# Kernel optimization log

Measured on AMD Instinct MI355X. Metric: run time of the kernel, lower is better.

The kernel has to match this reference:

```python
import jax, jax.numpy as jnp
import numpy as np
import math

D_MODEL = 1024
N_HEADS = 16
D_K = D_MODEL // N_HEADS
D_FF = 4096
B = 2
S = 2048
LN_EPS = 1e-3  # Keras LayerNormalization default


def setup_inputs() -> dict:
    key = jax.random.key(0)
    ks = jax.random.split(key, 16)
    s = 0.02
    inp = {
        "x": jax.random.normal(ks[0], (B, S, D_MODEL), dtype=jnp.float32),
        "weights": jax.random.uniform(ks[1], (B, S), dtype=jnp.float32),
        # attention projections (Dense: y = x @ W + b)
        "Wq": jax.random.normal(ks[2], (D_MODEL, D_MODEL), jnp.float32) * s,
        "bq": jnp.zeros((D_MODEL,), jnp.float32),
        "Wk": jax.random.normal(ks[3], (D_MODEL, D_MODEL), jnp.float32) * s,
        "bk": jnp.zeros((D_MODEL,), jnp.float32),
        "Wv": jax.random.normal(ks[4], (D_MODEL, D_MODEL), jnp.float32) * s,
        "bv": jnp.zeros((D_MODEL,), jnp.float32),
        "Wo": jax.random.normal(ks[5], (D_MODEL, D_MODEL), jnp.float32) * s,
        "bo": jnp.zeros((D_MODEL,), jnp.float32),
        # FFN
        "W1": jax.random.normal(ks[6], (D_MODEL, D_FF), jnp.float32) * s,
        "b1": jnp.zeros((D_FF,), jnp.float32),
        "W2": jax.random.normal(ks[7], (D_FF, D_MODEL), jnp.float32) * s,
        "b2": jnp.zeros((D_MODEL,), jnp.float32),
        # layer norms
        "g1": jnp.ones((D_MODEL,), jnp.float32),
        "be1": jnp.zeros((D_MODEL,), jnp.float32),
        "g2": jnp.ones((D_MODEL,), jnp.float32),
        "be2": jnp.zeros((D_MODEL,), jnp.float32),
    }
    return inp


def _layer_norm(x, gamma, beta):
    mu = jnp.mean(x, axis=-1, keepdims=True)
    var = jnp.mean(jnp.square(x - mu), axis=-1, keepdims=True)
    return (x - mu) * jax.lax.rsqrt(var + LN_EPS) * gamma + beta


def _block(x, weights, Wq, bq, Wk, bk, Wv, bv, Wo, bo, W1, b1, W2, b2, g1, be1, g2, be2):
    b, s, _ = x.shape
    # projections -> (B, H, S, d_k)
    def split_heads(y):
        return y.reshape(b, s, N_HEADS, D_K).transpose(0, 2, 1, 3)
    Q = split_heads(x @ Wq + bq)
    K = split_heads(x @ Wk + bk)
    V = split_heads(x @ Wv + bv)
    scores = jnp.einsum("bhqd,bhkd->bhqk", Q, K) / math.sqrt(D_K)
    log_w = jnp.log(weights + 1e-20)[:, None, None, :]  # (B,1,1,S)
    attn = jax.nn.softmax(scores + log_w, axis=-1)
    out = jnp.einsum("bhqk,bhkd->bhqd", attn, V)
    out = out.transpose(0, 2, 1, 3).reshape(b, s, D_MODEL)
    attn_out = out @ Wo + bo
    h = _layer_norm(x + attn_out, g1, be1)
    ffn = jax.nn.relu(h @ W1 + b1) @ W2 + b2
    return _layer_norm(h + ffn, g2, be2)


def reference(x, weights, Wq, bq, Wk, bk, Wv, bv, Wo, bo, W1, b1, W2, b2, g1, be1, g2, be2):
    return _block(x, weights, Wq, bq, Wk, bk, Wv, bv, Wo, bo, W1, b1, W2, b2, g1, be1, g2, be2)
```

## Files before the change

kernel.cpp:

```cpp
#include <hip/hip_runtime.h>
#include <cstdint>
#include <cstddef>

#define DM 1024
#define NH 16
#define DKH 64
#define DFF 4096
#define NB 2
#define SQL 2048
#define MROWS (NB * SQL)
#define QKVN 3072

typedef __attribute__((ext_vector_type(8))) __bf16 bf16x8;
typedef __attribute__((ext_vector_type(8))) short short8;
typedef __attribute__((ext_vector_type(4))) float f32x4;

__device__ __forceinline__ unsigned short f2bf(float f) {
    unsigned u = __float_as_uint(f);
    u += 0x7fffu + ((u >> 16) & 1u);
    return (unsigned short)(u >> 16);
}
__device__ __forceinline__ bf16x8 ldfrag(const unsigned short* p) {
    return __builtin_bit_cast(bf16x8, *(const short8*)p);
}
__device__ __forceinline__ void gl_lds16(const void* g, void* lds) {
    __builtin_amdgcn_global_load_lds(
        (const __attribute__((address_space(1))) unsigned int*)g,
        (__attribute__((address_space(3))) unsigned int*)lds, 16, 0, 0);
}
#define MFMA16(a, b, c) __builtin_amdgcn_mfma_f32_16x16x32_bf16(a, b, c, 0, 0, 0)

__global__ __launch_bounds__(256) void prep_misc(const float* __restrict__ x,
                                                 const float* __restrict__ wts,
                                                 const float* __restrict__ bq,
                                                 const float* __restrict__ bk,
                                                 const float* __restrict__ bv,
                                                 unsigned short* __restrict__ x_bf,
                                                 float* __restrict__ logw,
                                                 float* __restrict__ bqkv) {
    const int bid = blockIdx.x, tid = threadIdx.x;
    if (bid < 4096) {
        int i = (bid * 256 + tid) * 4;
        float4 v = *(const float4*)&x[i];
        ushort4 o;
        o.x = f2bf(v.x); o.y = f2bf(v.y); o.z = f2bf(v.z); o.w = f2bf(v.w);
        *(ushort4*)&x_bf[i] = o;
    } else if (bid < 4112) {
        int i = (bid - 4096) * 256 + tid;
        logw[i] = logf(wts[i] + 1e-20f);
    } else {
        int i = (bid - 4112) * 256 + tid;
        if (i < QKVN)
            bqkv[i] = i < 1024 ? bq[i] * 0.125f : (i < 2048 ? bk[i - 1024] : bv[i - 2048]);
    }
}

__global__ __launch_bounds__(256) void prep_weights(const float* __restrict__ Wq,
                                                    const float* __restrict__ Wk,
                                                    const float* __restrict__ Wv,
                                                    const float* __restrict__ Wo,
                                                    const float* __restrict__ W1,
                                                    unsigned short* __restrict__ wqkv_t,
                                                    unsigned short* __restrict__ Wo_t,
                                                    unsigned short* __restrict__ W1_t) {
    __shared__ float tile[32][33];
    const int t = blockIdx.x;
    const float* in;
    unsigned short* out;
    int K = DM, N = DM, n0, k0;
    float scale = 1.f;
    if (t < 1024)      { in = Wq; out = wqkv_t;                      scale = 0.125f;
                         n0 = (t & 31) * 32;          k0 = (t >> 5) * 32; }
    else if (t < 2048) { in = Wk; out = wqkv_t + (size_t)1024 * DM;
                         n0 = ((t - 1024) & 31) * 32; k0 = ((t - 1024) >> 5) * 32; }
    else if (t < 3072) { in = Wv; out = wqkv_t + (size_t)2048 * DM;
                         n0 = ((t - 2048) & 31) * 32; k0 = ((t - 2048) >> 5) * 32; }
    else if (t < 4096) { in = Wo; out = Wo_t;
                         n0 = ((t - 3072) & 31) * 32; k0 = ((t - 3072) >> 5) * 32; }
    else               { in = W1; out = W1_t; N = DFF;
                         n0 = ((t - 4096) & 127) * 32; k0 = ((t - 4096) >> 7) * 32; }
    const int tx = threadIdx.x & 31, ty = threadIdx.x >> 5;
#pragma unroll
    for (int i = 0; i < 32; i += 8)
        tile[ty + i][tx] = in[(size_t)(k0 + ty + i) * N + n0 + tx];
    __syncthreads();
#pragma unroll
    for (int i = 0; i < 32; i += 8)
        out[(size_t)(n0 + ty + i) * K + k0 + tx] = f2bf(tile[tx][ty + i] * scale);
}

__global__ __launch_bounds__(256) void transpose_f32_bf16(const float* __restrict__ in,
                                                          unsigned short* __restrict__ out,
                                                          int K, int N, float scale) {
    __shared__ float tile[32][33];
    const int n0 = blockIdx.x * 32, k0 = blockIdx.y * 32;
    const int tx = threadIdx.x & 31, ty = threadIdx.x >> 5;
#pragma unroll
    for (int i = 0; i < 32; i += 8)
        tile[ty + i][tx] = in[(size_t)(k0 + ty + i) * N + n0 + tx];
    __syncthreads();
#pragma unroll
    for (int i = 0; i < 32; i += 8)
        out[(size_t)(n0 + ty + i) * K + k0 + tx] = f2bf(tile[tx][ty + i] * scale);
}

template <int BN, bool RELU, int OMODE, int KSPL>
__global__ __launch_bounds__(256) void gemm_kernel(const unsigned short* __restrict__ A,
                                                   const unsigned short* __restrict__ Wt,
                                                   const float* __restrict__ bias,
                                                   void* __restrict__ outp,
                                                   unsigned short* __restrict__ vtp,
                                                   int M, int N, int K) {
    constexpr int NT = BN / 32;
    __shared__ unsigned short As[128 * 64];
    __shared__ unsigned short Bs[BN * 64];
    const int tid = threadIdx.x;
    const int wave = tid >> 6, lane = tid & 63;
    const int col16 = lane & 15, quad = lane >> 4;
    const int lrow = lane >> 3, sblk = (lane & 7) ^ (lrow & 7);
    const int m0 = blockIdx.y * 128, n0 = blockIdx.x * BN;
    const int wm = (wave >> 1) * 64, wn = (wave & 1) * (BN / 2);
    const int kbeg = (KSPL > 1) ? blockIdx.z * (K / KSPL) : 0;
    const int kend = kbeg + K / KSPL;

    f32x4 acc[4][NT] = {};

    for (int k0 = kbeg; k0 < kend; k0 += 64) {
        __syncthreads();
#pragma unroll
        for (int c = wave; c < 16; c += 4)
            gl_lds16(&A[(size_t)(m0 + c * 8 + lrow) * K + k0 + sblk * 8], &As[c * 512]);
#pragma unroll
        for (int c = wave; c < BN / 8; c += 4)
            gl_lds16(&Wt[(size_t)(n0 + c * 8 + lrow) * K + k0 + sblk * 8], &Bs[c * 512]);
        __syncthreads();
#pragma unroll
        for (int kk8 = 0; kk8 < 8; kk8 += 4) {
            bf16x8 af[4], bfr[NT];
#pragma unroll
            for (int t = 0; t < 4; ++t) {
                int R = wm + t * 16 + col16;
                af[t] = ldfrag(&As[R * 64 + (((kk8 + quad) ^ (R & 7)) << 3)]);
            }
#pragma unroll
            for (int t = 0; t < NT; ++t) {
                int R = wn + t * 16 + col16;
                bfr[t] = ldfrag(&Bs[R * 64 + (((kk8 + quad) ^ (R & 7)) << 3)]);
            }
#pragma unroll
            for (int mt = 0; mt < 4; ++mt)
#pragma unroll
                for (int nt = 0; nt < NT; ++nt)
                    acc[mt][nt] = MFMA16(af[mt], bfr[nt], acc[mt][nt]);
        }
    }

    float* outf = (float*)outp + ((KSPL > 1) ? (size_t)blockIdx.z * M * N : 0);
#pragma unroll
    for (int mt = 0; mt < 4; ++mt)
#pragma unroll
        for (int nt = 0; nt < NT; ++nt) {
            int col = n0 + wn + nt * 16 + col16;
            float bv = (KSPL == 1 || blockIdx.z == 0) ? bias[col] : 0.f;
            if (OMODE == 2 && col >= 2048) {
                int dl = (col - 2048) & 63, hh = (col - 2048) >> 6;
                int row0 = m0 + wm + mt * 16 + quad * 4;
                int bb = row0 >> 11, sb = row0 & 2047;
                ushort4 w4;
                w4.x = f2bf(acc[mt][nt][0] + bv);
                w4.y = f2bf(acc[mt][nt][1] + bv);
                w4.z = f2bf(acc[mt][nt][2] + bv);
                w4.w = f2bf(acc[mt][nt][3] + bv);
                *(ushort4*)&vtp[(size_t)(bb * NH + hh) * DKH * SQL + (size_t)dl * SQL + sb] = w4;
            } else {
#pragma unroll
                for (int r = 0; r < 4; ++r) {
                    int row = m0 + wm + mt * 16 + quad * 4 + r;
                    float v = acc[mt][nt][r] + bv;
                    if (RELU) v = fmaxf(v, 0.f);
                    if (OMODE == 0)
                        outf[(size_t)row * N + col] = v;
                    else
                        ((unsigned short*)outp)[(size_t)row * N + col] = f2bf(v);
                }
            }
        }
}

__global__ __launch_bounds__(256) void flash_kernel(const unsigned short* __restrict__ qkv,
                                                    const unsigned short* __restrict__ vt,
                                                    const float* __restrict__ logw,
                                                    float* __restrict__ po,
                                                    float* __restrict__ pl) {
    __shared__ unsigned short Ks[64 * 64];
    __shared__ unsigned short Vt[64 * 64];
    __shared__ unsigned short Ps[4][16][72];
    __shared__ float lws[64];

    const int tid = threadIdx.x, wave = tid >> 6, lane = tid & 63;
    const int col16 = lane & 15, quad = lane >> 4;
    const int lrow = lane >> 3, sblk = (lane & 7) ^ (lrow & 7);
    const int bh = blockIdx.y, b = bh >> 4, h = bh & 15;
    const int q0 = blockIdx.x * 64;
    const int split = blockIdx.z;

    const unsigned short* Kg = qkv + (size_t)b * SQL * QKVN + 1024 + h * DKH;
    const unsigned short* Vg = vt + (size_t)bh * DKH * SQL;

    bf16x8 qf[2];
    {
        const unsigned short* qrow =
            qkv + (size_t)(b * SQL + q0 + wave * 16 + col16) * QKVN + h * DKH;
        qf[0] = ldfrag(qrow + quad * 8);
        qf[1] = ldfrag(qrow + 32 + quad * 8);
    }
    bf16x8 ones;
    {
        short8 o8 = {0x3f80, 0x3f80, 0x3f80, 0x3f80, 0x3f80, 0x3f80, 0x3f80, 0x3f80};
        ones = __builtin_bit_cast(bf16x8, o8);
    }

    f32x4 o[4] = {};
    f32x4 lacc = {};

    for (int kt = split * (SQL / 2); kt < (split + 1) * (SQL / 2); kt += 64) {
        __syncthreads();
#pragma unroll
        for (int c = wave; c < 8; c += 4) {
            gl_lds16(&Kg[(size_t)(kt + c * 8 + lrow) * QKVN + sblk * 8], &Ks[c * 512]);
            gl_lds16(&Vg[(size_t)(c * 8 + lrow) * SQL + kt + sblk * 8], &Vt[c * 512]);
        }
        if (tid < 64) lws[tid] = logw[b * SQL + kt + tid];
        __syncthreads();

        float pv[4][4];
#pragma unroll
        for (int nt = 0; nt < 4; ++nt) {
            int R = nt * 16 + col16;
            f32x4 s4 = {};
            s4 = MFMA16(qf[0], ldfrag(&Ks[R * 64 + ((quad ^ (R & 7)) << 3)]), s4);
            s4 = MFMA16(qf[1], ldfrag(&Ks[R * 64 + (((4 + quad) ^ (R & 7)) << 3)]), s4);
            float lw = lws[R];
#pragma unroll
            for (int r = 0; r < 4; ++r) pv[nt][r] = __expf(s4[r] + lw);
        }
#pragma unroll
        for (int nt = 0; nt < 4; ++nt)
#pragma unroll
            for (int r = 0; r < 4; ++r)
                Ps[wave][quad * 4 + r][nt * 16 + col16] = f2bf(pv[nt][r]);
        __syncthreads();

#pragma unroll
        for (int kk8 = 0; kk8 < 8; kk8 += 4) {
            bf16x8 psf = ldfrag(&Ps[wave][col16][(kk8 + quad) << 3]);
            lacc = MFMA16(ones, psf, lacc);
#pragma unroll
            for (int dt = 0; dt < 4; ++dt) {
                int R = dt * 16 + col16;
                bf16x8 vf = ldfrag(&Vt[R * 64 + (((kk8 + quad) ^ (R & 7)) << 3)]);
                o[dt] = MFMA16(vf, psf, o[dt]);
            }
        }
    }

    const size_t prow = (size_t)(split * 32 + bh) * SQL + q0 + wave * 16 + col16;
#pragma unroll
    for (int dt = 0; dt < 4; ++dt) {
        float4 v4 = {o[dt][0], o[dt][1], o[dt][2], o[dt][3]};
        *(float4*)&po[prow * 64 + dt * 16 + quad * 4] = v4;
    }
    if (quad == 0) pl[prow] = lacc[0];
}

__global__ __launch_bounds__(256) void combine_kernel(const float* __restrict__ po,
                                                      const float* __restrict__ pl,
                                                      unsigned short* __restrict__ attn_bf) {
    const int gid = blockIdx.x * 256 + threadIdx.x;
    const int t = gid & 15;
    const int row = gid >> 4;
    const int bh = row >> 11, q = row & 2047;
    const int b = bh >> 4, h = bh & 15;
    float4 a = *(const float4*)&po[(size_t)row * 64 + t * 4];
    float4 c = *(const float4*)&po[(size_t)(row + 65536) * 64 + t * 4];
    float rl = 1.f / (pl[row] + pl[row + 65536]);
    ushort4 o;
    o.x = f2bf((a.x + c.x) * rl);
    o.y = f2bf((a.y + c.y) * rl);
    o.z = f2bf((a.z + c.z) * rl);
    o.w = f2bf((a.w + c.w) * rl);
    *(ushort4*)&attn_bf[(size_t)(b * SQL + q) * DM + h * DKH + t * 4] = o;
}

__global__ __launch_bounds__(256) void ln1_kernel(const float* __restrict__ x,
                                                  const float* __restrict__ d0,
                                                  const float* __restrict__ d1,
                                                  const float* __restrict__ g,
                                                  const float* __restrict__ be,
                                                  float* __restrict__ hf,
                                                  unsigned short* __restrict__ hb) {
    const int row = blockIdx.x, tid = threadIdx.x;
    float4 xv = *(const float4*)&x[(size_t)row * DM + tid * 4];
    float4 av = *(const float4*)&d0[(size_t)row * DM + tid * 4];
    float4 bv = *(const float4*)&d1[(size_t)row * DM + tid * 4];
    float v[4] = {xv.x + av.x + bv.x, xv.y + av.y + bv.y, xv.z + av.z + bv.z,
                  xv.w + av.w + bv.w};
    float s = v[0] + v[1] + v[2] + v[3];
    float ss = v[0] * v[0] + v[1] * v[1] + v[2] * v[2] + v[3] * v[3];
#pragma unroll
    for (int m = 1; m < 64; m <<= 1) { s += __shfl_xor(s, m); ss += __shfl_xor(ss, m); }
    __shared__ float sb[4], ssb[4];
    if ((tid & 63) == 0) { sb[tid >> 6] = s; ssb[tid >> 6] = ss; }
    __syncthreads();
    s = sb[0] + sb[1] + sb[2] + sb[3];
    ss = ssb[0] + ssb[1] + ssb[2] + ssb[3];
    float mu = s * (1.f / DM);
    float var = fmaxf(ss * (1.f / DM) - mu * mu, 0.f);
    float rs = rsqrtf(var + 1e-3f);
#pragma unroll
    for (int i = 0; i < 4; ++i) {
        int c = tid * 4 + i;
        float y = (v[i] - mu) * rs * g[c] + be[c];
        hf[(size_t)row * DM + c] = y;
        hb[(size_t)row * DM + c] = f2bf(y);
    }
}

__global__ __launch_bounds__(256) void ln2_kernel(const float* __restrict__ hf,
                                                  const float* __restrict__ d0,
                                                  const float* __restrict__ d1,
                                                  const float* __restrict__ g,
                                                  const float* __restrict__ be,
                                                  float* __restrict__ outp) {
    const int row = blockIdx.x, tid = threadIdx.x;
    float4 hv = *(const float4*)&hf[(size_t)row * DM + tid * 4];
    float4 av = *(const float4*)&d0[(size_t)row * DM + tid * 4];
    float4 bv = *(const float4*)&d1[(size_t)row * DM + tid * 4];
    float v[4] = {hv.x + av.x + bv.x, hv.y + av.y + bv.y, hv.z + av.z + bv.z,
                  hv.w + av.w + bv.w};
    float s = v[0] + v[1] + v[2] + v[3];
    float ss = v[0] * v[0] + v[1] * v[1] + v[2] * v[2] + v[3] * v[3];
#pragma unroll
    for (int m = 1; m < 64; m <<= 1) { s += __shfl_xor(s, m); ss += __shfl_xor(ss, m); }
    __shared__ float sb[4], ssb[4];
    if ((tid & 63) == 0) { sb[tid >> 6] = s; ssb[tid >> 6] = ss; }
    __syncthreads();
    s = sb[0] + sb[1] + sb[2] + sb[3];
    ss = ssb[0] + ssb[1] + ssb[2] + ssb[3];
    float mu = s * (1.f / DM);
    float var = fmaxf(ss * (1.f / DM) - mu * mu, 0.f);
    float rs = rsqrtf(var + 1e-3f);
    float4 ov;
    ov.x = (v[0] - mu) * rs * g[tid * 4 + 0] + be[tid * 4 + 0];
    ov.y = (v[1] - mu) * rs * g[tid * 4 + 1] + be[tid * 4 + 1];
    ov.z = (v[2] - mu) * rs * g[tid * 4 + 2] + be[tid * 4 + 2];
    ov.w = (v[3] - mu) * rs * g[tid * 4 + 3] + be[tid * 4 + 3];
    *(float4*)&outp[(size_t)row * DM + tid * 4] = ov;
}

extern "C" void kernel_launch(void* const* d_in, const int* in_sizes, int n_in,
                              void* d_out, int out_size, void* d_ws, size_t ws_size,
                              hipStream_t stream) {
    const float* x   = (const float*)d_in[0];
    const float* wts = (const float*)d_in[1];
    const float* Wq  = (const float*)d_in[2];
    const float* bq  = (const float*)d_in[3];
    const float* Wk  = (const float*)d_in[4];
    const float* bk  = (const float*)d_in[5];
    const float* Wv  = (const float*)d_in[6];
    const float* bv  = (const float*)d_in[7];
    const float* Wo  = (const float*)d_in[8];
    const float* bo  = (const float*)d_in[9];
    const float* W1  = (const float*)d_in[10];
    const float* b1  = (const float*)d_in[11];
    const float* W2  = (const float*)d_in[12];
    const float* b2  = (const float*)d_in[13];
    const float* g1  = (const float*)d_in[14];
    const float* be1 = (const float*)d_in[15];
    const float* g2  = (const float*)d_in[16];
    const float* be2 = (const float*)d_in[17];

    char* ws = (char*)d_ws;
    const size_t MB = 1u << 20;
    unsigned short* qkv_bf  = (unsigned short*)(ws + 0 * MB);
    unsigned short* vt      = (unsigned short*)(ws + 24 * MB);
    unsigned short* x_bf    = (unsigned short*)(ws + 32 * MB);
    unsigned short* wqkv_t  = (unsigned short*)(ws + 40 * MB);
    unsigned short* Wo_t    = (unsigned short*)(ws + 46 * MB);
    unsigned short* W1_t    = (unsigned short*)(ws + 48 * MB);
    float* po               = (float*)(ws + 64 * MB);
    unsigned short* W2_t    = (unsigned short*)(ws + 88 * MB);
    float* pl               = (float*)(ws + 98 * MB);
    float* bqkv             = (float*)(ws + 98 * MB + 0x80000);
    float* logw             = (float*)(ws + 98 * MB + 0x88000);
    unsigned short* attn_bf = (unsigned short*)(ws + 32 * MB);
    float* attnproj         = (float*)(ws + 0 * MB);
    float* h_f32            = (float*)(ws + 64 * MB);
    unsigned short* h_bf    = (unsigned short*)(ws + 80 * MB);
    unsigned short* ffn1_bf = (unsigned short*)(ws + 0 * MB);
    float* ffn2             = (float*)(ws + 32 * MB);

    prep_misc<<<4124, 256, 0, stream>>>(x, wts, bq, bk, bv, x_bf, logw, bqkv);
    prep_weights<<<8192, 256, 0, stream>>>(Wq, Wk, Wv, Wo, W1, wqkv_t, Wo_t, W1_t);

    gemm_kernel<128, false, 2, 1><<<dim3(QKVN / 128, MROWS / 128), 256, 0, stream>>>(
        x_bf, wqkv_t, bqkv, qkv_bf, vt, MROWS, QKVN, DM);

    flash_kernel<<<dim3(SQL / 64, NB * NH, 2), 256, 0, stream>>>(qkv_bf, vt, logw, po, pl);
    combine_kernel<<<(32 * 2048 * 16) / 256, 256, 0, stream>>>(po, pl, attn_bf);

    transpose_f32_bf16<<<dim3(32, 128), 256, 0, stream>>>(W2, W2_t, DFF, DM, 1.f);

    gemm_kernel<128, false, 0, 2><<<dim3(DM / 128, MROWS / 128, 2), 256, 0, stream>>>(
        attn_bf, Wo_t, bo, attnproj, nullptr, MROWS, DM, DM);
    ln1_kernel<<<MROWS, 256, 0, stream>>>(x, attnproj, attnproj + (size_t)MROWS * DM,
                                          g1, be1, h_f32, h_bf);

    gemm_kernel<128, true, 1, 1><<<dim3(DFF / 128, MROWS / 128), 256, 0, stream>>>(
        h_bf, W1_t, b1, ffn1_bf, nullptr, MROWS, DFF, DM);
    gemm_kernel<128, false, 0, 2><<<dim3(DM / 128, MROWS / 128, 2), 256, 0, stream>>>(
        ffn1_bf, W2_t, b2, ffn2, nullptr, MROWS, DM, DFF);
    ln2_kernel<<<MROWS, 256, 0, stream>>>(h_f32, ffn2, ffn2 + (size_t)MROWS * DM,
                                          g2, be2, (float*)d_out);
}
```

Baseline: 386.0 us.

## Drop flash split-K combine, use 512-thread flash blocks, fold W2 transpose

The flash attention kernel no longer splits the key range in two. It now uses 512-thread blocks covering 128 queries and normalizes and writes bf16 output directly, so the separate combine kernel and the fp32 partial-output round trip are gone. The W2 transpose is merged into the prep_weights launch, and the two N=1024 GEMMs switch to BN=64 tiles, which doubles the block count. The trade-off is that flash now launches fewer, longer blocks (512 vs 2048 before) with no key-split parallelism, which may hurt occupancy.

```diff
diff --git a/kernel.cpp b/kernel.cpp
--- a/kernel.cpp
+++ b/kernel.cpp
@@ -60,9 +60,11 @@
                                                     const float* __restrict__ Wv,
                                                     const float* __restrict__ Wo,
                                                     const float* __restrict__ W1,
+                                                    const float* __restrict__ W2,
                                                     unsigned short* __restrict__ wqkv_t,
                                                     unsigned short* __restrict__ Wo_t,
-                                                    unsigned short* __restrict__ W1_t) {
+                                                    unsigned short* __restrict__ W1_t,
+                                                    unsigned short* __restrict__ W2_t) {
     __shared__ float tile[32][33];
     const int t = blockIdx.x;
     const float* in;
@@ -77,23 +79,10 @@
                          n0 = ((t - 2048) & 31) * 32; k0 = ((t - 2048) >> 5) * 32; }
     else if (t < 4096) { in = Wo; out = Wo_t;
                          n0 = ((t - 3072) & 31) * 32; k0 = ((t - 3072) >> 5) * 32; }
-    else               { in = W1; out = W1_t; N = DFF;
+    else if (t < 8192) { in = W1; out = W1_t; N = DFF;
                          n0 = ((t - 4096) & 127) * 32; k0 = ((t - 4096) >> 7) * 32; }
-    const int tx = threadIdx.x & 31, ty = threadIdx.x >> 5;
-#pragma unroll
-    for (int i = 0; i < 32; i += 8)
-        tile[ty + i][tx] = in[(size_t)(k0 + ty + i) * N + n0 + tx];
-    __syncthreads();
-#pragma unroll
-    for (int i = 0; i < 32; i += 8)
-        out[(size_t)(n0 + ty + i) * K + k0 + tx] = f2bf(tile[tx][ty + i] * scale);
-}
-
-__global__ __launch_bounds__(256) void transpose_f32_bf16(const float* __restrict__ in,
-                                                          unsigned short* __restrict__ out,
-                                                          int K, int N, float scale) {
-    __shared__ float tile[32][33];
-    const int n0 = blockIdx.x * 32, k0 = blockIdx.y * 32;
+    else               { in = W2; out = W2_t; K = DFF;
+                         n0 = ((t - 8192) & 31) * 32;  k0 = ((t - 8192) >> 5) * 32; }
     const int tx = threadIdx.x & 31, ty = threadIdx.x >> 5;
 #pragma unroll
     for (int i = 0; i < 32; i += 8)
@@ -187,22 +176,20 @@
         }
 }
 
-__global__ __launch_bounds__(256) void flash_kernel(const unsigned short* __restrict__ qkv,
+__global__ __launch_bounds__(512) void flash_kernel(const unsigned short* __restrict__ qkv,
                                                     const unsigned short* __restrict__ vt,
                                                     const float* __restrict__ logw,
-                                                    float* __restrict__ po,
-                                                    float* __restrict__ pl) {
+                                                    unsigned short* __restrict__ attn_bf) {
     __shared__ unsigned short Ks[64 * 64];
     __shared__ unsigned short Vt[64 * 64];
-    __shared__ unsigned short Ps[4][16][72];
+    __shared__ unsigned short Ps[8][16][72];
     __shared__ float lws[64];
 
     const int tid = threadIdx.x, wave = tid >> 6, lane = tid & 63;
     const int col16 = lane & 15, quad = lane >> 4;
     const int lrow = lane >> 3, sblk = (lane & 7) ^ (lrow & 7);
     const int bh = blockIdx.y, b = bh >> 4, h = bh & 15;
-    const int q0 = blockIdx.x * 64;
-    const int split = blockIdx.z;
+    const int q0 = blockIdx.x * 128;
 
     const unsigned short* Kg = qkv + (size_t)b * SQL * QKVN + 1024 + h * DKH;
     const unsigned short* Vg = vt + (size_t)bh * DKH * SQL;
@@ -223,10 +210,10 @@
     f32x4 o[4] = {};
     f32x4 lacc = {};
 
-    for (int kt = split * (SQL / 2); kt < (split + 1) * (SQL / 2); kt += 64) {
-        __syncthreads();
-#pragma unroll
-        for (int c = wave; c < 8; c += 4) {
+    for (int kt = 0; kt < SQL; kt += 64) {
+        __syncthreads();
+        if (wave < 8) {
+            int c = wave;
             gl_lds16(&Kg[(size_t)(kt + c * 8 + lrow) * QKVN + sblk * 8], &Ks[c * 512]);
             gl_lds16(&Vg[(size_t)(c * 8 + lrow) * SQL + kt + sblk * 8], &Vt[c * 512]);
         }
@@ -264,32 +251,17 @@
         }
     }
 
-    const size_t prow = (size_t)(split * 32 + bh) * SQL + q0 + wave * 16 + col16;
+    const float rl = 1.0f / lacc[0];
+    const int qrow = b * SQL + q0 + wave * 16 + col16;
 #pragma unroll
     for (int dt = 0; dt < 4; ++dt) {
-        float4 v4 = {o[dt][0], o[dt][1], o[dt][2], o[dt][3]};
-        *(float4*)&po[prow * 64 + dt * 16 + quad * 4] = v4;
-    }
-    if (quad == 0) pl[prow] = lacc[0];
-}
-
-__global__ __launch_bounds__(256) void combine_kernel(const float* __restrict__ po,
-                                                      const float* __restrict__ pl,
-                                                      unsigned short* __restrict__ attn_bf) {
-    const int gid = blockIdx.x * 256 + threadIdx.x;
-    const int t = gid & 15;
-    const int row = gid >> 4;
-    const int bh = row >> 11, q = row & 2047;
-    const int b = bh >> 4, h = bh & 15;
-    float4 a = *(const float4*)&po[(size_t)row * 64 + t * 4];
-    float4 c = *(const float4*)&po[(size_t)(row + 65536) * 64 + t * 4];
-    float rl = 1.f / (pl[row] + pl[row + 65536]);
-    ushort4 o;
-    o.x = f2bf((a.x + c.x) * rl);
-    o.y = f2bf((a.y + c.y) * rl);
-    o.z = f2bf((a.z + c.z) * rl);
-    o.w = f2bf((a.w + c.w) * rl);
-    *(ushort4*)&attn_bf[(size_t)(b * SQL + q) * DM + h * DKH + t * 4] = o;
+        ushort4 h4;
+        h4.x = f2bf(o[dt][0] * rl);
+        h4.y = f2bf(o[dt][1] * rl);
+        h4.z = f2bf(o[dt][2] * rl);
+        h4.w = f2bf(o[dt][3] * rl);
+        *(ushort4*)&attn_bf[(size_t)qrow * DM + h * DKH + dt * 16 + quad * 4] = h4;
+    }
 }
 
 __global__ __launch_bounds__(256) void ln1_kernel(const float* __restrict__ x,
@@ -388,37 +360,33 @@
     unsigned short* wqkv_t  = (unsigned short*)(ws + 40 * MB);
     unsigned short* Wo_t    = (unsigned short*)(ws + 46 * MB);
     unsigned short* W1_t    = (unsigned short*)(ws + 48 * MB);
-    float* po               = (float*)(ws + 64 * MB);
+    float* h_f32            = (float*)(ws + 64 * MB);
+    unsigned short* h_bf    = (unsigned short*)(ws + 80 * MB);
     unsigned short* W2_t    = (unsigned short*)(ws + 88 * MB);
-    float* pl               = (float*)(ws + 98 * MB);
-    float* bqkv             = (float*)(ws + 98 * MB + 0x80000);
-    float* logw             = (float*)(ws + 98 * MB + 0x88000);
+    float* bqkv             = (float*)(ws + 96 * MB);
+    float* logw             = (float*)(ws + 96 * MB + 0x8000);
     unsigned short* attn_bf = (unsigned short*)(ws + 32 * MB);
     float* attnproj         = (float*)(ws + 0 * MB);
-    float* h_f32            = (float*)(ws + 64 * MB);
-    unsigned short* h_bf    = (unsigned short*)(ws + 80 * MB);
     unsigned short* ffn1_bf = (unsigned short*)(ws + 0 * MB);
     float* ffn2             = (float*)(ws + 32 * MB);
 
     prep_misc<<<4124, 256, 0, stream>>>(x, wts, bq, bk, bv, x_bf, logw, bqkv);
-    prep_weights<<<8192, 256, 0, stream>>>(Wq, Wk, Wv, Wo, W1, wqkv_t, Wo_t, W1_t);
+    prep_weights<<<12288, 256, 0, stream>>>(Wq, Wk, Wv, Wo, W1, W2,
+                                            wqkv_t, Wo_t, W1_t, W2_t);
 
     gemm_kernel<128, false, 2, 1><<<dim3(QKVN / 128, MROWS / 128), 256, 0, stream>>>(
         x_bf, wqkv_t, bqkv, qkv_bf, vt, MROWS, QKVN, DM);
 
-    flash_kernel<<<dim3(SQL / 64, NB * NH, 2), 256, 0, stream>>>(qkv_bf, vt, logw, po, pl);
-    combine_kernel<<<(32 * 2048 * 16) / 256, 256, 0, stream>>>(po, pl, attn_bf);
-
-    transpose_f32_bf16<<<dim3(32, 128), 256, 0, stream>>>(W2, W2_t, DFF, DM, 1.f);
-
-    gemm_kernel<128, false, 0, 2><<<dim3(DM / 128, MROWS / 128, 2), 256, 0, stream>>>(
+    flash_kernel<<<dim3(SQL / 128, NB * NH), 512, 0, stream>>>(qkv_bf, vt, logw, attn_bf);
+
+    gemm_kernel<64, false, 0, 2><<<dim3(DM / 64, MROWS / 128, 2), 256, 0, stream>>>(
         attn_bf, Wo_t, bo, attnproj, nullptr, MROWS, DM, DM);
     ln1_kernel<<<MROWS, 256, 0, stream>>>(x, attnproj, attnproj + (size_t)MROWS * DM,
                                           g1, be1, h_f32, h_bf);
 
     gemm_kernel<128, true, 1, 1><<<dim3(DFF / 128, MROWS / 128), 256, 0, stream>>>(
         h_bf, W1_t, b1, ffn1_bf, nullptr, MROWS, DFF, DM);
-    gemm_kernel<128, false, 0, 2><<<dim3(DM / 128, MROWS / 128, 2), 256, 0, stream>>>(
+    gemm_kernel<64, false, 0, 2><<<dim3(DM / 64, MROWS / 128, 2), 256, 0, stream>>>(
         ffn1_bf, W2_t, b2, ffn2, nullptr, MROWS, DM, DFF);
     ln2_kernel<<<MROWS, 256, 0, stream>>>(h_f32, ffn2, ffn2 + (size_t)MROWS * DM,
                                           g2, be2, (float*)d_out);
```

Result: faster. 356.7 us (-7.6%).
